# Performance work log

Measured on AMD Instinct MI355X. Metric: run time of the kernel, lower is better.

Reference implementation:

```python
import jax, jax.numpy as jnp
import numpy as np

N_NODES = 50000
N_EDGES = 800000
NEG_SLOPE = 0.2


def _gat_layer(x, src, dst, W, a_src, a_dst, b, heads, out_ch, num_nodes):
    # Linear projection per head: [N, H, C]
    h = (x @ W).reshape(num_nodes, heads, out_ch)
    # Per-node attention logits [N, H]
    al_src = jnp.sum(h * a_src, axis=-1)
    al_dst = jnp.sum(h * a_dst, axis=-1)
    # Per-edge scores, LeakyReLU as in PyG GATConv: alpha_j (src) + alpha_i (dst)
    e = jax.nn.leaky_relu(al_src[src] + al_dst[dst], NEG_SLOPE)  # [E, H]
    # Segment softmax over incoming edges of each destination node
    m = jax.ops.segment_max(e, dst, num_segments=num_nodes)       # [N, H]
    e = jnp.exp(e - m[dst])
    denom = jax.ops.segment_sum(e, dst, num_segments=num_nodes)   # [N, H]
    alpha = e / (denom[dst] + 1e-16)                              # [E, H]
    # Attention-weighted aggregation: scatter-add messages to destinations
    out = jax.ops.segment_sum(h[src] * alpha[:, :, None], dst, num_segments=num_nodes)
    return out.reshape(num_nodes, heads * out_ch) + b


def _forward(x, edge_index, W1, a_src1, a_dst1, b1, W2, a_src2, a_dst2, b2, W3, a_src3, a_dst3, b3):
    n = x.shape[0]
    loops = jnp.arange(n, dtype=edge_index.dtype)
    src = jnp.concatenate([edge_index[0], loops])
    dst = jnp.concatenate([edge_index[1], loops])
    h = _gat_layer(x, src, dst, W1, a_src1, a_dst1, b1, 4, 64, n)
    h = jax.nn.elu(h)
    h = _gat_layer(h, src, dst, W2, a_src2, a_dst2, b2, 2, 64, n)
    h = jax.nn.elu(h)
    h = _gat_layer(h, src, dst, W3, a_src3, a_dst3, b3, 1, 16, n)
    return jax.nn.log_softmax(h, axis=1)


def setup_inputs() -> dict:
    key = jax.random.key(0)
    ks = jax.random.split(key, 12)
    s = lambda fan: 1.0 / np.sqrt(fan)
    return {
        "x": jax.random.normal(ks[0], (N_NODES, 128), dtype=jnp.float32),
        "edge_index": jax.random.randint(ks[1], (2, N_EDGES), 0, N_NODES, dtype=jnp.int64),
        "W1": jax.random.normal(ks[2], (128, 256), dtype=jnp.float32) * s(128),
        "a_src1": jax.random.normal(ks[3], (4, 64), dtype=jnp.float32) * s(64),
        "a_dst1": jax.random.normal(ks[4], (4, 64), dtype=jnp.float32) * s(64),
        "b1": jnp.zeros((256,), dtype=jnp.float32),
        "W2": jax.random.normal(ks[5], (256, 128), dtype=jnp.float32) * s(256),
        "a_src2": jax.random.normal(ks[6], (2, 64), dtype=jnp.float32) * s(64),
        "a_dst2": jax.random.normal(ks[7], (2, 64), dtype=jnp.float32) * s(64),
        "b2": jnp.zeros((128,), dtype=jnp.float32),
        "W3": jax.random.normal(ks[8], (128, 16), dtype=jnp.float32) * s(128),
        "a_src3": jax.random.normal(ks[9], (1, 16), dtype=jnp.float32) * s(16),
        "a_dst3": jax.random.normal(ks[10], (1, 16), dtype=jnp.float32) * s(16),
        "b3": jnp.zeros((16,), dtype=jnp.float32),
    }


def reference(x, edge_index, W1, a_src1, a_dst1, b1, W2, a_src2, a_dst2, b2, W3, a_src3, a_dst3, b3):
    return _forward(x, edge_index, W1, a_src1, a_dst1, b1, W2, a_src2, a_dst2, b2, W3, a_src3, a_dst3, b3)
```

## Files before the change

### kernel.cpp

```cpp
#include <hip/hip_runtime.h>
#include <math.h>


#define NEG_SLOPE 0.2f

typedef __attribute__((ext_vector_type(8))) short short8;
typedef __attribute__((ext_vector_type(4))) float f32x4;

__device__ inline unsigned short f2bf(float f) {
    union { float f; unsigned u; } c{f};
    unsigned r = (c.u + 0x7FFFu + ((c.u >> 16) & 1u)) >> 16;
    return (unsigned short)r;
}
__device__ inline float bflo(unsigned u) {
    union { unsigned u; float f; } c{u << 16};
    return c.f;
}
__device__ inline float bfhi(unsigned u) {
    union { unsigned u; float f; } c{u & 0xFFFF0000u};
    return c.f;
}
__device__ inline float bf2f(unsigned short v) {
    union { unsigned u; float f; } c{(unsigned)v << 16};
    return c.f;
}

__global__ __launch_bounds__(256) void detect_kernel(const unsigned int* __restrict__ w,
                                                     int* __restrict__ flag) {
    __shared__ int nz;
    if (threadIdx.x == 0) nz = 0;
    __syncthreads();
    unsigned int v = w[2 * threadIdx.x + 1];
    if (v != 0) atomicAdd(&nz, 1);
    __syncthreads();
    if (threadIdx.x == 0) *flag = (nz == 0) ? 1 : 0;
}

__global__ __launch_bounds__(256) void convert_kernel(const unsigned int* __restrict__ w,
                                                      const int* __restrict__ flag,
                                                      int* __restrict__ src32,
                                                      int* __restrict__ dst32,
                                                      int* __restrict__ counts,
                                                      int E, int NN) {
    int i = blockIdx.x * 256 + threadIdx.x;
    int total = E + NN;
    if (i >= total) return;
    int is64 = *flag;
    int s, d;
    if (i < E) {
        if (is64) {
            s = (int)w[2 * (size_t)i];
            d = (int)w[2 * ((size_t)E + i)];
        } else {
            s = (int)w[i];
            d = (int)w[E + i];
        }
    } else {
        s = d = i - E;
    }
    src32[i] = s;
    dst32[i] = d;
    atomicAdd(&counts[d], 1);
}

__global__ __launch_bounds__(256) void scan_partial(const int* __restrict__ counts,
                                                    int* __restrict__ bsum, int n) {
    int i = blockIdx.x * 256 + threadIdx.x;
    int v = (i < n) ? counts[i] : 0;
    for (int d = 1; d < 64; d <<= 1) v += __shfl_xor(v, d);
    __shared__ int ws[4];
    if ((threadIdx.x & 63) == 0) ws[threadIdx.x >> 6] = v;
    __syncthreads();
    if (threadIdx.x == 0) bsum[blockIdx.x] = ws[0] + ws[1] + ws[2] + ws[3];
}

__global__ __launch_bounds__(1024) void scan_bsum(int* __restrict__ bsum, int nb) {
    __shared__ int s[1024];
    int t = threadIdx.x;
    int v = (t < nb) ? bsum[t] : 0;
    s[t] = v;
    __syncthreads();
    for (int d = 1; d < 1024; d <<= 1) {
        int u = (t >= d) ? s[t - d] : 0;
        __syncthreads();
        s[t] += u;
        __syncthreads();
    }
    if (t < nb) bsum[t] = s[t] - v;
}

__global__ __launch_bounds__(256) void scan_write(const int* __restrict__ counts,
                                                  const int* __restrict__ bsum,
                                                  int* __restrict__ offsets,
                                                  int* __restrict__ cursor, int n) {
    int i = blockIdx.x * 256 + threadIdx.x;
    int v = (i < n) ? counts[i] : 0;
    int lane = threadIdx.x & 63, w = threadIdx.x >> 6;
    int sc = v;
    for (int d = 1; d < 64; d <<= 1) {
        int u = __shfl_up(sc, d);
        if (lane >= d) sc += u;
    }
    __shared__ int wsum[4];
    if (lane == 63) wsum[w] = sc;
    __syncthreads();
    int base = bsum[blockIdx.x];
    for (int j = 0; j < w; ++j) base += wsum[j];
    int excl = base + sc - v;
    if (i < n) {
        offsets[i] = excl;
        cursor[i] = excl;
        if (i == n - 1) offsets[n] = excl + v;
    }
}

__global__ __launch_bounds__(256) void scatter_kernel(const int* __restrict__ src32,
                                                      const int* __restrict__ dst32,
                                                      int* __restrict__ cursor,
                                                      int* __restrict__ csr_src,
                                                      int total) {
    int i = blockIdx.x * 256 + threadIdx.x;
    if (i >= total) return;
    int d = dst32[i];
    int pos = atomicAdd(&cursor[d], 1);
    csr_src[pos] = src32[i];
}

__global__ __launch_bounds__(256) void prep_kernel(const float* __restrict__ x,
                                                   const float* __restrict__ W1,
                                                   const float* __restrict__ W2,
                                                   const float* __restrict__ W3,
                                                   unsigned short* __restrict__ xbf,
                                                   unsigned short* __restrict__ WT1,
                                                   unsigned short* __restrict__ WT2,
                                                   unsigned short* __restrict__ WT3,
                                                   int xn4) {
    int i = blockIdx.x * 256 + threadIdx.x;
    if (i < xn4) {
        float4 v = reinterpret_cast<const float4*>(x)[i];
        ushort4 o;
        o.x = f2bf(v.x); o.y = f2bf(v.y); o.z = f2bf(v.z); o.w = f2bf(v.w);
        reinterpret_cast<ushort4*>(xbf)[i] = o;
        return;
    }
    int j = i - xn4;
    if (j < 128 * 256) {
        int k = j / 256, n = j % 256;
        WT1[(size_t)n * 128 + k] = f2bf(W1[j]);
        return;
    }
    j -= 128 * 256;
    if (j < 256 * 128) {
        int k = j / 128, n = j % 128;
        WT2[(size_t)n * 256 + k] = f2bf(W2[j]);
        return;
    }
    j -= 256 * 128;
    if (j < 128 * 16) {
        int k = j / 16, n = j % 16;
        WT3[(size_t)n * 128 + k] = f2bf(W3[j]);
    }
}

template <int K, int N, int C>
__global__ __launch_bounds__(256) void gemm_mfma_al(const unsigned short* __restrict__ Xbf,
                                                    const unsigned short* __restrict__ WT,
                                                    unsigned short* __restrict__ Hbf,
                                                    const float* __restrict__ a_src,
                                                    const float* __restrict__ a_dst,
                                                    float* __restrict__ alS,
                                                    float* __restrict__ alD,
                                                    int M) {
    constexpr int KK = K / 32;
    constexpr int HH = N / C;
    constexpr int SEG = C / 16;
    int wave = threadIdx.x >> 6;
    int lane = threadIdx.x & 63;
    int row0 = blockIdx.x * 64 + wave * 16;
    int rowA = row0 + (lane & 15);
    int kb = (lane >> 4) * 8;
    short8 a[KK];
    if (rowA < M) {
#pragma unroll
        for (int kk = 0; kk < KK; ++kk)
            a[kk] = *reinterpret_cast<const short8*>(&Xbf[(size_t)rowA * K + kk * 32 + kb]);
    } else {
#pragma unroll
        for (int kk = 0; kk < KK; ++kk)
            a[kk] = short8{0, 0, 0, 0, 0, 0, 0, 0};
    }
    int col = lane & 15;
    int rbase = row0 + ((lane >> 4) << 2);
    bool full = (rbase + 3) < M;
    float ps[4] = {0.f, 0.f, 0.f, 0.f};
    float pd[4] = {0.f, 0.f, 0.f, 0.f};
#pragma unroll
    for (int nc = 0; nc < N / 16; ++nc) {
        f32x4 acc = {0.f, 0.f, 0.f, 0.f};
#pragma unroll
        for (int kk = 0; kk < KK; ++kk) {
            short8 b = *reinterpret_cast<const short8*>(&WT[(size_t)(nc * 16 + col) * K + kk * 32 + kb]);
            acc = __builtin_amdgcn_mfma_f32_16x16x32_bf16(a[kk], b, acc, 0, 0, 0);
        }
        int j = nc * 16 + col;
        float asj = a_src[j], adj = a_dst[j];
#pragma unroll
        for (int r = 0; r < 4; ++r) {
            unsigned short hb = f2bf(acc[r]);
            if (full || (rbase + r < M))
                Hbf[(size_t)(rbase + r) * N + j] = hb;
            float hv = bf2f(hb);
            ps[r] = fmaf(hv, asj, ps[r]);
            pd[r] = fmaf(hv, adj, pd[r]);
        }
        if ((nc % SEG) == SEG - 1) {
            int head = nc / SEG;
#pragma unroll
            for (int r = 0; r < 4; ++r) {
                for (int d = 1; d < 16; d <<= 1) {
                    ps[r] += __shfl_xor(ps[r], d);
                    pd[r] += __shfl_xor(pd[r], d);
                }
            }
            if ((lane & 15) == 0) {
#pragma unroll
                for (int r = 0; r < 4; ++r) {
                    if (rbase + r < M) {
                        alS[(size_t)(rbase + r) * HH + head] = ps[r];
                        alD[(size_t)(rbase + r) * HH + head] = pd[r];
                    }
                }
            }
#pragma unroll
            for (int r = 0; r < 4; ++r) { ps[r] = 0.f; pd[r] = 0.f; }
        }
    }
}

template <int H>
__global__ __launch_bounds__(256) void softmax_kernel(const float* __restrict__ alS,
                                                      const float* __restrict__ alD,
                                                      const int* __restrict__ offsets,
                                                      const int* __restrict__ csr_src,
                                                      float* __restrict__ pbuf,
                                                      float* __restrict__ rsbuf) {
    int li = threadIdx.x & 15;
    int node = blockIdx.x * 16 + (threadIdx.x >> 4);
    int beg = offsets[node];
    int end = offsets[node + 1];
    float ad[H];
#pragma unroll
    for (int h = 0; h < H; ++h) ad[h] = alD[(size_t)node * H + h];

    float m[H];
#pragma unroll
    for (int h = 0; h < H; ++h) m[h] = -INFINITY;

    for (int i = beg + li; i < end; i += 16) {
        int sn = csr_src[i];
        float e[H];
        if constexpr (H == 4) {
            float4 v = *reinterpret_cast<const float4*>(&alS[(size_t)sn * 4]);
            e[0] = v.x; e[1] = v.y; e[2] = v.z; e[3] = v.w;
        } else if constexpr (H == 2) {
            float2 v = *reinterpret_cast<const float2*>(&alS[(size_t)sn * 2]);
            e[0] = v.x; e[1] = v.y;
        } else {
            e[0] = alS[sn];
        }
#pragma unroll
        for (int h = 0; h < H; ++h) {
            e[h] += ad[h];
            e[h] = (e[h] > 0.f) ? e[h] : NEG_SLOPE * e[h];
            m[h] = fmaxf(m[h], e[h]);
        }
        if constexpr (H == 4) {
            *reinterpret_cast<float4*>(&pbuf[(size_t)i * 4]) = make_float4(e[0], e[1], e[2], e[3]);
        } else if constexpr (H == 2) {
            *reinterpret_cast<float2*>(&pbuf[(size_t)i * 2]) = make_float2(e[0], e[1]);
        } else {
            pbuf[i] = e[0];
        }
    }
#pragma unroll
    for (int h = 0; h < H; ++h)
        for (int d = 1; d < 16; d <<= 1) m[h] = fmaxf(m[h], __shfl_xor(m[h], d, 16));

    float s[H];
#pragma unroll
    for (int h = 0; h < H; ++h) s[h] = 0.f;
    for (int i = beg + li; i < end; i += 16) {
        float p[H];
        if constexpr (H == 4) {
            float4 v = *reinterpret_cast<const float4*>(&pbuf[(size_t)i * 4]);
            p[0] = v.x; p[1] = v.y; p[2] = v.z; p[3] = v.w;
        } else if constexpr (H == 2) {
            float2 v = *reinterpret_cast<const float2*>(&pbuf[(size_t)i * 2]);
            p[0] = v.x; p[1] = v.y;
        } else {
            p[0] = pbuf[i];
        }
#pragma unroll
        for (int h = 0; h < H; ++h) {
            p[h] = __expf(p[h] - m[h]);
            s[h] += p[h];
        }
        if constexpr (H == 4) {
            *reinterpret_cast<float4*>(&pbuf[(size_t)i * 4]) = make_float4(p[0], p[1], p[2], p[3]);
        } else if constexpr (H == 2) {
            *reinterpret_cast<float2*>(&pbuf[(size_t)i * 2]) = make_float2(p[0], p[1]);
        } else {
            pbuf[i] = p[0];
        }
    }
#pragma unroll
    for (int h = 0; h < H; ++h)
        for (int d = 1; d < 16; d <<= 1) s[h] += __shfl_xor(s[h], d, 16);

    if (li == 0) {
#pragma unroll
        for (int h = 0; h < H; ++h)
            rsbuf[(size_t)node * H + h] = 1.f / (s[h] + 1e-16f);
    }
}

template <int H, int C, int ACT>
__global__ __launch_bounds__(256) void agg8_kernel(const unsigned short* __restrict__ hbf,
                                                   const float* __restrict__ pbuf,
                                                   const float* __restrict__ rsbuf,
                                                   const int* __restrict__ offsets,
                                                   const int* __restrict__ csr_src,
                                                   const float* __restrict__ bias,
                                                   unsigned short* __restrict__ outbf,
                                                   float* __restrict__ outf,
                                                   int NN) {
    constexpr int HC = H * C;
    constexpr int HC8 = HC / 8;
    constexpr int NPB = 256 / HC8;
    int g = threadIdx.x / HC8;
    int l8 = threadIdx.x % HC8;
    int hd = (l8 * 8) / C;
    int node = blockIdx.x * NPB + g;
    if (node >= NN) return;
    int beg = offsets[node];
    int end = offsets[node + 1];
    const uint4* __restrict__ h4 = reinterpret_cast<const uint4*>(hbf);

    float acc[8];
#pragma unroll
    for (int k = 0; k < 8; ++k) acc[k] = 0.f;

    int i = beg;
    for (; i + 4 <= end; i += 4) {
        int sn0 = csr_src[i + 0];
        int sn1 = csr_src[i + 1];
        int sn2 = csr_src[i + 2];
        int sn3 = csr_src[i + 3];
        float p0 = pbuf[(size_t)(i + 0) * H + hd];
        float p1 = pbuf[(size_t)(i + 1) * H + hd];
        float p2 = pbuf[(size_t)(i + 2) * H + hd];
        float p3 = pbuf[(size_t)(i + 3) * H + hd];
        uint4 v0 = h4[(size_t)sn0 * HC8 + l8];
        uint4 v1 = h4[(size_t)sn1 * HC8 + l8];
        uint4 v2 = h4[(size_t)sn2 * HC8 + l8];
        uint4 v3 = h4[(size_t)sn3 * HC8 + l8];
#define ACC8(vv, pp)                                        \
        acc[0] = fmaf(pp, bflo(vv.x), acc[0]);              \
        acc[1] = fmaf(pp, bfhi(vv.x), acc[1]);              \
        acc[2] = fmaf(pp, bflo(vv.y), acc[2]);              \
        acc[3] = fmaf(pp, bfhi(vv.y), acc[3]);              \
        acc[4] = fmaf(pp, bflo(vv.z), acc[4]);              \
        acc[5] = fmaf(pp, bfhi(vv.z), acc[5]);              \
        acc[6] = fmaf(pp, bflo(vv.w), acc[6]);              \
        acc[7] = fmaf(pp, bfhi(vv.w), acc[7]);
        ACC8(v0, p0)
        ACC8(v1, p1)
        ACC8(v2, p2)
        ACC8(v3, p3)
    }
    for (; i < end; ++i) {
        int sn = csr_src[i];
        float p = pbuf[(size_t)i * H + hd];
        uint4 v = h4[(size_t)sn * HC8 + l8];
        ACC8(v, p)
    }
#undef ACC8

    float rs = rsbuf[(size_t)node * H + hd];
    float val[8];
#pragma unroll
    for (int k = 0; k < 8; ++k)
        val[k] = acc[k] * rs + bias[l8 * 8 + k];
    if constexpr (ACT == 1) {
#pragma unroll
        for (int k = 0; k < 8; ++k)
            val[k] = (val[k] > 0.f) ? val[k] : expm1f(val[k]);
        uint4 o;
        o.x = (unsigned)f2bf(val[0]) | ((unsigned)f2bf(val[1]) << 16);
        o.y = (unsigned)f2bf(val[2]) | ((unsigned)f2bf(val[3]) << 16);
        o.z = (unsigned)f2bf(val[4]) | ((unsigned)f2bf(val[5]) << 16);
        o.w = (unsigned)f2bf(val[6]) | ((unsigned)f2bf(val[7]) << 16);
        reinterpret_cast<uint4*>(outbf)[(size_t)node * HC8 + l8] = o;
    }
    if constexpr (ACT == 2) {
        float mx = val[0];
#pragma unroll
        for (int k = 1; k < 8; ++k) mx = fmaxf(mx, val[k]);
        mx = fmaxf(mx, __shfl_xor(mx, 1, 2));
        float sm = 0.f;
#pragma unroll
        for (int k = 0; k < 8; ++k) sm += __expf(val[k] - mx);
        sm += __shfl_xor(sm, 1, 2);
        float lg = mx + logf(sm);
#pragma unroll
        for (int k = 0; k < 8; ++k) val[k] -= lg;
        float4* o4 = reinterpret_cast<float4*>(outf) + (size_t)node * (HC / 4) + l8 * 2;
        o4[0] = make_float4(val[0], val[1], val[2], val[3]);
        o4[1] = make_float4(val[4], val[5], val[6], val[7]);
    }
}

extern "C" void kernel_launch(void* const* d_in, const int* in_sizes, int n_in,
                              void* d_out, int out_size, void* d_ws, size_t ws_size,
                              hipStream_t stream) {
    const float* x = (const float*)d_in[0];
    const unsigned int* ei = (const unsigned int*)d_in[1];
    const float* W1 = (const float*)d_in[2];
    const float* as1 = (const float*)d_in[3];
    const float* ad1 = (const float*)d_in[4];
    const float* b1 = (const float*)d_in[5];
    const float* W2 = (const float*)d_in[6];
    const float* as2 = (const float*)d_in[7];
    const float* ad2 = (const float*)d_in[8];
    const float* b2 = (const float*)d_in[9];
    const float* W3 = (const float*)d_in[10];
    const float* as3 = (const float*)d_in[11];
    const float* ad3 = (const float*)d_in[12];
    const float* b3 = (const float*)d_in[13];
    float* out = (float*)d_out;

    const int NN = in_sizes[0] / 128;
    const int E = in_sizes[1] / 2;
    const int TOT = E + NN;

    char* base = (char*)d_ws;
    size_t off = 0;
    auto take = [&](size_t bytes) -> void* {
        void* p = base + off;
        off += (bytes + 255) & ~(size_t)255;
        return p;
    };
    int* flag = (int*)take(4);
    int* offsets = (int*)take((size_t)(NN + 1) * 4);
    int* csr_src = (int*)take((size_t)TOT * 4);
    float* alS = (float*)take((size_t)NN * 4 * 4);
    float* alD = (float*)take((size_t)NN * 4 * 4);
    float* rsbuf = (float*)take((size_t)NN * 4 * 4);
    unsigned short* xbf = (unsigned short*)take((size_t)NN * 128 * 2);
    unsigned short* hbf = (unsigned short*)take((size_t)NN * 256 * 2);
    unsigned short* aggbf = (unsigned short*)take((size_t)NN * 256 * 2);
    unsigned short* WT1 = (unsigned short*)take(256 * 128 * 2);
    unsigned short* WT2 = (unsigned short*)take(128 * 256 * 2);
    unsigned short* WT3 = (unsigned short*)take(16 * 128 * 2);
    int* bsum = (int*)take(1024 * 4);
    size_t build_bytes = (size_t)TOT * 4 * 2 + (size_t)NN * 4 * 2 + 1024;
    size_t pbuf_bytes = (size_t)TOT * 4 * 4;
    char* ov = (char*)take(build_bytes > pbuf_bytes ? build_bytes : pbuf_bytes);
    int* src32 = (int*)ov;
    int* dst32 = src32 + TOT;
    int* counts = dst32 + TOT;
    int* cursor = counts + NN;
    float* pbuf = (float*)ov;
    (void)ws_size;

    int egrid = (TOT + 255) / 256;
    int sgrid = (NN + 255) / 256;
    int ggrid = (NN + 63) / 64;
    int smgrid = (NN + 15) / 16;
    int grid_agg1 = NN / 8;
    int grid_agg2 = NN / 16;
    int grid_agg3 = (NN + 127) / 128;
    int xn4 = NN * 128 / 4;
    int prep_total = xn4 + 128 * 256 + 256 * 128 + 128 * 16;

    prep_kernel<<<(prep_total + 255) / 256, 256, 0, stream>>>(x, W1, W2, W3, xbf, WT1, WT2, WT3, xn4);
    detect_kernel<<<1, 256, 0, stream>>>(ei, flag);
    hipMemsetAsync(counts, 0, (size_t)NN * 4, stream);
    convert_kernel<<<egrid, 256, 0, stream>>>(ei, flag, src32, dst32, counts, E, NN);
    scan_partial<<<sgrid, 256, 0, stream>>>(counts, bsum, NN);
    scan_bsum<<<1, 1024, 0, stream>>>(bsum, sgrid);
    scan_write<<<sgrid, 256, 0, stream>>>(counts, bsum, offsets, cursor, NN);
    scatter_kernel<<<egrid, 256, 0, stream>>>(src32, dst32, cursor, csr_src, TOT);

    gemm_mfma_al<128, 256, 64><<<ggrid, 256, 0, stream>>>(xbf, WT1, hbf, as1, ad1, alS, alD, NN);
    softmax_kernel<4><<<smgrid, 256, 0, stream>>>(alS, alD, offsets, csr_src, pbuf, rsbuf);
    agg8_kernel<4, 64, 1><<<grid_agg1, 256, 0, stream>>>(hbf, pbuf, rsbuf, offsets, csr_src, b1, aggbf, nullptr, NN);

    gemm_mfma_al<256, 128, 64><<<ggrid, 256, 0, stream>>>(aggbf, WT2, hbf, as2, ad2, alS, alD, NN);
    softmax_kernel<2><<<smgrid, 256, 0, stream>>>(alS, alD, offsets, csr_src, pbuf, rsbuf);
    agg8_kernel<2, 64, 1><<<grid_agg2, 256, 0, stream>>>(hbf, pbuf, rsbuf, offsets, csr_src, b2, aggbf, nullptr, NN);

    gemm_mfma_al<128, 16, 16><<<ggrid, 256, 0, stream>>>(aggbf, WT3, hbf, as3, ad3, alS, alD, NN);
    softmax_kernel<1><<<smgrid, 256, 0, stream>>>(alS, alD, offsets, csr_src, pbuf, rsbuf);
    agg8_kernel<1, 16, 2><<<grid_agg3, 256, 0, stream>>>(hbf, pbuf, rsbuf, offsets, csr_src, b3, nullptr, out, NN);
}
```

Before: 413.9 us.

## Fuse edge softmax into aggregation kernel and drop the per-edge probability buffer

Removes the separate softmax kernel for each layer. The aggregation kernel now computes each edge's leaky-ReLU logit and exponent inline from alS/alD, accumulates the normalizer alongside the weighted sum, and divides at the end. This eliminates three launches and the write and re-read of the per-edge probability buffer. The trade-off is that the max subtraction is dropped, so large logits could overflow exp, and every thread of a head recomputes the exponent redundantly.

```diff
diff --git a/kernel.cpp b/kernel.cpp
--- a/kernel.cpp
+++ b/kernel.cpp
@@ -237,97 +237,10 @@
     }
 }
 
-template <int H>
-__global__ __launch_bounds__(256) void softmax_kernel(const float* __restrict__ alS,
-                                                      const float* __restrict__ alD,
-                                                      const int* __restrict__ offsets,
-                                                      const int* __restrict__ csr_src,
-                                                      float* __restrict__ pbuf,
-                                                      float* __restrict__ rsbuf) {
-    int li = threadIdx.x & 15;
-    int node = blockIdx.x * 16 + (threadIdx.x >> 4);
-    int beg = offsets[node];
-    int end = offsets[node + 1];
-    float ad[H];
-#pragma unroll
-    for (int h = 0; h < H; ++h) ad[h] = alD[(size_t)node * H + h];
-
-    float m[H];
-#pragma unroll
-    for (int h = 0; h < H; ++h) m[h] = -INFINITY;
-
-    for (int i = beg + li; i < end; i += 16) {
-        int sn = csr_src[i];
-        float e[H];
-        if constexpr (H == 4) {
-            float4 v = *reinterpret_cast<const float4*>(&alS[(size_t)sn * 4]);
-            e[0] = v.x; e[1] = v.y; e[2] = v.z; e[3] = v.w;
-        } else if constexpr (H == 2) {
-            float2 v = *reinterpret_cast<const float2*>(&alS[(size_t)sn * 2]);
-            e[0] = v.x; e[1] = v.y;
-        } else {
-            e[0] = alS[sn];
-        }
-#pragma unroll
-        for (int h = 0; h < H; ++h) {
-            e[h] += ad[h];
-            e[h] = (e[h] > 0.f) ? e[h] : NEG_SLOPE * e[h];
-            m[h] = fmaxf(m[h], e[h]);
-        }
-        if constexpr (H == 4) {
-            *reinterpret_cast<float4*>(&pbuf[(size_t)i * 4]) = make_float4(e[0], e[1], e[2], e[3]);
-        } else if constexpr (H == 2) {
-            *reinterpret_cast<float2*>(&pbuf[(size_t)i * 2]) = make_float2(e[0], e[1]);
-        } else {
-            pbuf[i] = e[0];
-        }
-    }
-#pragma unroll
-    for (int h = 0; h < H; ++h)
-        for (int d = 1; d < 16; d <<= 1) m[h] = fmaxf(m[h], __shfl_xor(m[h], d, 16));
-
-    float s[H];
-#pragma unroll
-    for (int h = 0; h < H; ++h) s[h] = 0.f;
-    for (int i = beg + li; i < end; i += 16) {
-        float p[H];
-        if constexpr (H == 4) {
-            float4 v = *reinterpret_cast<const float4*>(&pbuf[(size_t)i * 4]);
-            p[0] = v.x; p[1] = v.y; p[2] = v.z; p[3] = v.w;
-        } else if constexpr (H == 2) {
-            float2 v = *reinterpret_cast<const float2*>(&pbuf[(size_t)i * 2]);
-            p[0] = v.x; p[1] = v.y;
-        } else {
-            p[0] = pbuf[i];
-        }
-#pragma unroll
-        for (int h = 0; h < H; ++h) {
-            p[h] = __expf(p[h] - m[h]);
-            s[h] += p[h];
-        }
-        if constexpr (H == 4) {
-            *reinterpret_cast<float4*>(&pbuf[(size_t)i * 4]) = make_float4(p[0], p[1], p[2], p[3]);
-        } else if constexpr (H == 2) {
-            *reinterpret_cast<float2*>(&pbuf[(size_t)i * 2]) = make_float2(p[0], p[1]);
-        } else {
-            pbuf[i] = p[0];
-        }
-    }
-#pragma unroll
-    for (int h = 0; h < H; ++h)
-        for (int d = 1; d < 16; d <<= 1) s[h] += __shfl_xor(s[h], d, 16);
-
-    if (li == 0) {
-#pragma unroll
-        for (int h = 0; h < H; ++h)
-            rsbuf[(size_t)node * H + h] = 1.f / (s[h] + 1e-16f);
-    }
-}
-
 template <int H, int C, int ACT>
-__global__ __launch_bounds__(256) void agg8_kernel(const unsigned short* __restrict__ hbf,
-                                                   const float* __restrict__ pbuf,
-                                                   const float* __restrict__ rsbuf,
+__global__ __launch_bounds__(256) void aggf_kernel(const unsigned short* __restrict__ hbf,
+                                                   const float* __restrict__ alS,
+                                                   const float* __restrict__ alD,
                                                    const int* __restrict__ offsets,
                                                    const int* __restrict__ csr_src,
                                                    const float* __restrict__ bias,
@@ -344,26 +257,20 @@
     if (node >= NN) return;
     int beg = offsets[node];
     int end = offsets[node + 1];
+    float ad = alD[(size_t)node * H + hd];
     const uint4* __restrict__ h4 = reinterpret_cast<const uint4*>(hbf);
 
     float acc[8];
 #pragma unroll
     for (int k = 0; k < 8; ++k) acc[k] = 0.f;
-
-    int i = beg;
-    for (; i + 4 <= end; i += 4) {
-        int sn0 = csr_src[i + 0];
-        int sn1 = csr_src[i + 1];
-        int sn2 = csr_src[i + 2];
-        int sn3 = csr_src[i + 3];
-        float p0 = pbuf[(size_t)(i + 0) * H + hd];
-        float p1 = pbuf[(size_t)(i + 1) * H + hd];
-        float p2 = pbuf[(size_t)(i + 2) * H + hd];
-        float p3 = pbuf[(size_t)(i + 3) * H + hd];
-        uint4 v0 = h4[(size_t)sn0 * HC8 + l8];
-        uint4 v1 = h4[(size_t)sn1 * HC8 + l8];
-        uint4 v2 = h4[(size_t)sn2 * HC8 + l8];
-        uint4 v3 = h4[(size_t)sn3 * HC8 + l8];
+    float s = 0.f;
+
+#define EDGE_P(sn, pv)                                      \
+    {                                                       \
+        float e_ = alS[(size_t)(sn) * H + hd] + ad;         \
+        e_ = (e_ > 0.f) ? e_ : NEG_SLOPE * e_;              \
+        pv = __expf(e_);                                    \
+    }
 #define ACC8(vv, pp)                                        \
         acc[0] = fmaf(pp, bflo(vv.x), acc[0]);              \
         acc[1] = fmaf(pp, bfhi(vv.x), acc[1]);              \
@@ -373,6 +280,23 @@
         acc[5] = fmaf(pp, bfhi(vv.z), acc[5]);              \
         acc[6] = fmaf(pp, bflo(vv.w), acc[6]);              \
         acc[7] = fmaf(pp, bfhi(vv.w), acc[7]);
+
+    int i = beg;
+    for (; i + 4 <= end; i += 4) {
+        int sn0 = csr_src[i + 0];
+        int sn1 = csr_src[i + 1];
+        int sn2 = csr_src[i + 2];
+        int sn3 = csr_src[i + 3];
+        uint4 v0 = h4[(size_t)sn0 * HC8 + l8];
+        uint4 v1 = h4[(size_t)sn1 * HC8 + l8];
+        uint4 v2 = h4[(size_t)sn2 * HC8 + l8];
+        uint4 v3 = h4[(size_t)sn3 * HC8 + l8];
+        float p0, p1, p2, p3;
+        EDGE_P(sn0, p0)
+        EDGE_P(sn1, p1)
+        EDGE_P(sn2, p2)
+        EDGE_P(sn3, p3)
+        s += (p0 + p1) + (p2 + p3);
         ACC8(v0, p0)
         ACC8(v1, p1)
         ACC8(v2, p2)
@@ -380,13 +304,16 @@
     }
     for (; i < end; ++i) {
         int sn = csr_src[i];
-        float p = pbuf[(size_t)i * H + hd];
         uint4 v = h4[(size_t)sn * HC8 + l8];
+        float p;
+        EDGE_P(sn, p)
+        s += p;
         ACC8(v, p)
     }
 #undef ACC8
-
-    float rs = rsbuf[(size_t)node * H + hd];
+#undef EDGE_P
+
+    float rs = 1.f / (s + 1e-16f);
     float val[8];
 #pragma unroll
     for (int k = 0; k < 8; ++k)
@@ -455,7 +382,6 @@
     int* csr_src = (int*)take((size_t)TOT * 4);
     float* alS = (float*)take((size_t)NN * 4 * 4);
     float* alD = (float*)take((size_t)NN * 4 * 4);
-    float* rsbuf = (float*)take((size_t)NN * 4 * 4);
     unsigned short* xbf = (unsigned short*)take((size_t)NN * 128 * 2);
     unsigned short* hbf = (unsigned short*)take((size_t)NN * 256 * 2);
     unsigned short* aggbf = (unsigned short*)take((size_t)NN * 256 * 2);
@@ -463,20 +389,15 @@
     unsigned short* WT2 = (unsigned short*)take(128 * 256 * 2);
     unsigned short* WT3 = (unsigned short*)take(16 * 128 * 2);
     int* bsum = (int*)take(1024 * 4);
-    size_t build_bytes = (size_t)TOT * 4 * 2 + (size_t)NN * 4 * 2 + 1024;
-    size_t pbuf_bytes = (size_t)TOT * 4 * 4;
-    char* ov = (char*)take(build_bytes > pbuf_bytes ? build_bytes : pbuf_bytes);
-    int* src32 = (int*)ov;
-    int* dst32 = src32 + TOT;
-    int* counts = dst32 + TOT;
-    int* cursor = counts + NN;
-    float* pbuf = (float*)ov;
+    int* src32 = (int*)take((size_t)TOT * 4);
+    int* dst32 = (int*)take((size_t)TOT * 4);
+    int* counts = (int*)take((size_t)NN * 4);
+    int* cursor = (int*)take((size_t)NN * 4);
     (void)ws_size;
 
     int egrid = (TOT + 255) / 256;
     int sgrid = (NN + 255) / 256;
     int ggrid = (NN + 63) / 64;
-    int smgrid = (NN + 15) / 16;
     int grid_agg1 = NN / 8;
     int grid_agg2 = NN / 16;
     int grid_agg3 = (NN + 127) / 128;
@@ -493,14 +414,11 @@
     scatter_kernel<<<egrid, 256, 0, stream>>>(src32, dst32, cursor, csr_src, TOT);
 
     gemm_mfma_al<128, 256, 64><<<ggrid, 256, 0, stream>>>(xbf, WT1, hbf, as1, ad1, alS, alD, NN);
-    softmax_kernel<4><<<smgrid, 256, 0, stream>>>(alS, alD, offsets, csr_src, pbuf, rsbuf);
-    agg8_kernel<4, 64, 1><<<grid_agg1, 256, 0, stream>>>(hbf, pbuf, rsbuf, offsets, csr_src, b1, aggbf, nullptr, NN);
+    aggf_kernel<4, 64, 1><<<grid_agg1, 256, 0, stream>>>(hbf, alS, alD, offsets, csr_src, b1, aggbf, nullptr, NN);
 
     gemm_mfma_al<256, 128, 64><<<ggrid, 256, 0, stream>>>(aggbf, WT2, hbf, as2, ad2, alS, alD, NN);
-    softmax_kernel<2><<<smgrid, 256, 0, stream>>>(alS, alD, offsets, csr_src, pbuf, rsbuf);
-    agg8_kernel<2, 64, 1><<<grid_agg2, 256, 0, stream>>>(hbf, pbuf, rsbuf, offsets, csr_src, b2, aggbf, nullptr, NN);
+    aggf_kernel<2, 64, 1><<<grid_agg2, 256, 0, stream>>>(hbf, alS, alD, offsets, csr_src, b2, aggbf, nullptr, NN);
 
     gemm_mfma_al<128, 16, 16><<<ggrid, 256, 0, stream>>>(aggbf, WT3, hbf, as3, ad3, alS, alD, NN);
-    softmax_kernel<1><<<smgrid, 256, 0, stream>>>(alS, alD, offsets, csr_src, pbuf, rsbuf);
-    agg8_kernel<1, 16, 2><<<grid_agg3, 256, 0, stream>>>(hbf, pbuf, rsbuf, offsets, csr_src, b3, nullptr, out, NN);
-}
+    aggf_kernel<1, 16, 2><<<grid_agg3, 256, 0, stream>>>(hbf, alS, alD, offsets, csr_src, b3, nullptr, out, NN);
+}
```

Measured after the change: 391.3 us. 5.5% less time.
